# Performance work log

Hardware: AMD Instinct MI355X
Metric: run time of the kernel (lower is better)

Reference implementation:

```python
import jax, jax.numpy as jnp
import numpy as np

IN_F = 4096
OUT_F = 4096
BITS = 8
EPS = 1e-5
BATCH, SEQ = 4, 2048


def setup_inputs() -> dict:
    key = jax.random.key(0)
    k1, k2, k3 = jax.random.split(key, 3)
    bound = 1.0 / np.sqrt(IN_F)
    x = jax.random.normal(k1, (BATCH, SEQ, IN_F), dtype=jnp.float32)
    weight = jax.random.uniform(k2, (OUT_F, IN_F), dtype=jnp.float32, minval=-bound, maxval=bound)
    bias = jax.random.uniform(k3, (OUT_F,), dtype=jnp.float32, minval=-bound, maxval=bound)
    return {"x": x, "weight": weight, "bias": bias}


def _ste_round_clip(v, lo, hi):
    # round+clip with straight-through estimator
    q = jnp.clip(jnp.round(v), lo, hi)
    return v + jax.lax.stop_gradient(q - v)


def reference(x, weight, bias):
    q = jnp.float32(2 ** (BITS - 1))  # 128 for int8
    # weight ternarization: absmean scale, round to {-1,0,1}
    w_scale = jnp.maximum(jnp.mean(jnp.abs(weight)), EPS)
    w_q = _ste_round_clip(weight / w_scale, -1.0, 1.0)  # ternary [O,I]
    # activation int8 quantization: absmax scale over whole tensor (dim=None)
    gamma = jnp.maximum(jnp.max(jnp.abs(x)), EPS)
    x_q = _ste_round_clip(x * (q / gamma), -q, q - 1.0)  # int8 range values
    # integer-domain matmul then dequantize
    out = jnp.einsum('bsi,oi->bso', x_q, w_q) * (gamma * w_scale / q)
    return out + bias
```

## Files before the change

kernel.cpp:

```cpp
#include <hip/hip_runtime.h>
#include <stdint.h>

#define GLOBAL_AS __attribute__((address_space(1)))
#define LDS_AS __attribute__((address_space(3)))

typedef int v4i  __attribute__((ext_vector_type(4)));
typedef int v16i __attribute__((ext_vector_type(16)));

static constexpr int M = 8192;
static constexpr int N = 4096;
static constexpr int K = 4096;
static constexpr float F_EPS = 1e-5f;


__global__ void reduce_kernel(const float4* __restrict__ x, const float4* __restrict__ w,
                              float* __restrict__ pmax, double* __restrict__ psum) {
    const int b = blockIdx.x;
    const int t = threadIdx.x;
    if (b < 2048) {
        float m = 0.f;
        const int n4 = M * K / 4;
        int i = b * 512 + t;
        for (; i + 256 < n4; i += 2048 * 512) {
            float4 v0 = x[i];
            float4 v1 = x[i + 256];
            m = fmaxf(m, fmaxf(fmaxf(fabsf(v0.x), fabsf(v0.y)), fmaxf(fabsf(v0.z), fabsf(v0.w))));
            m = fmaxf(m, fmaxf(fmaxf(fabsf(v1.x), fabsf(v1.y)), fmaxf(fabsf(v1.z), fabsf(v1.w))));
        }
#pragma unroll
        for (int off = 32; off > 0; off >>= 1) m = fmaxf(m, __shfl_down(m, off, 64));
        __shared__ float red[4];
        if ((t & 63) == 0) red[t >> 6] = m;
        __syncthreads();
        if (t == 0) pmax[b] = fmaxf(fmaxf(red[0], red[1]), fmaxf(red[2], red[3]));
    } else {
        double s = 0.0;
        const int n4 = N * K / 4;
        int i = (b - 2048) * 512 + t;
        for (; i + 256 < n4; i += 1024 * 512) {
            float4 v0 = w[i];
            float4 v1 = w[i + 256];
            s += (double)fabsf(v0.x) + (double)fabsf(v0.y) + (double)fabsf(v0.z) + (double)fabsf(v0.w);
            s += (double)fabsf(v1.x) + (double)fabsf(v1.y) + (double)fabsf(v1.z) + (double)fabsf(v1.w);
        }
#pragma unroll
        for (int off = 32; off > 0; off >>= 1) s += __shfl_down(s, off, 64);
        __shared__ double dred[4];
        if ((t & 63) == 0) dred[t >> 6] = s;
        __syncthreads();
        if (t == 0) psum[b - 2048] = dred[0] + dred[1] + dred[2] + dred[3];
    }
}

__global__ void quant_kernel(const float4* __restrict__ x, const float4* __restrict__ w,
                             int* __restrict__ xq, int* __restrict__ wq,
                             const float* __restrict__ pmax, const double* __restrict__ psum,
                             float* __restrict__ wssc) {
    const int b = blockIdx.x;
    const int t = threadIdx.x;
    __shared__ float red[4];
    __shared__ double dred[4];
    __shared__ float sc[2];
    {
        float m = 0.f;
#pragma unroll
        for (int j = 0; j < 8; ++j) m = fmaxf(m, pmax[t + j * 256]);
        double s = psum[t] + psum[t + 256] + psum[t + 512] + psum[t + 768];
#pragma unroll
        for (int off = 32; off > 0; off >>= 1) {
            m = fmaxf(m, __shfl_down(m, off, 64));
            s += __shfl_down(s, off, 64);
        }
        if ((t & 63) == 0) { red[t >> 6] = m; dred[t >> 6] = s; }
        __syncthreads();
        if (t == 0) {
            float gamma = fmaxf(fmaxf(fmaxf(red[0], red[1]), fmaxf(red[2], red[3])), F_EPS);
            double sum = dred[0] + dred[1] + dred[2] + dred[3];
            float wscale = (float)fmax(sum * (1.0 / ((double)N * (double)K)), (double)F_EPS);
            sc[0] = 128.f / gamma;
            sc[1] = wscale;
            if (b == 0) {
                wssc[0] = 128.f / gamma;
                wssc[1] = wscale;
                wssc[2] = gamma * wscale / 128.f;
            }
        }
        __syncthreads();
    }
    const float sx = sc[0];
    const float ws = sc[1];

    if (b < 2048) {
        const int n4 = M * K / 4;
        int i = b * 512 + t;
        for (; i + 256 < n4; i += 2048 * 512) {
            float4 v0 = x[i];
            float4 v1 = x[i + 256];
            int a0 = min(127, max(-128, (int)rintf(v0.x * sx)));
            int a1 = min(127, max(-128, (int)rintf(v0.y * sx)));
            int a2 = min(127, max(-128, (int)rintf(v0.z * sx)));
            int a3 = min(127, max(-128, (int)rintf(v0.w * sx)));
            xq[i] = (a0 & 255) | ((a1 & 255) << 8) | ((a2 & 255) << 16) | (a3 << 24);
            int b0 = min(127, max(-128, (int)rintf(v1.x * sx)));
            int b1 = min(127, max(-128, (int)rintf(v1.y * sx)));
            int b2 = min(127, max(-128, (int)rintf(v1.z * sx)));
            int b3 = min(127, max(-128, (int)rintf(v1.w * sx)));
            xq[i + 256] = (b0 & 255) | ((b1 & 255) << 8) | ((b2 & 255) << 16) | (b3 << 24);
        }
    } else {
        const int n4 = N * K / 4;
        int i = (b - 2048) * 512 + t;
        for (; i + 256 < n4; i += 1024 * 512) {
            float4 v0 = w[i];
            float4 v1 = w[i + 256];
            int a0 = min(1, max(-1, (int)rintf(v0.x / ws)));
            int a1 = min(1, max(-1, (int)rintf(v0.y / ws)));
            int a2 = min(1, max(-1, (int)rintf(v0.z / ws)));
            int a3 = min(1, max(-1, (int)rintf(v0.w / ws)));
            wq[i] = (a0 & 255) | ((a1 & 255) << 8) | ((a2 & 255) << 16) | (a3 << 24);
            int b0 = min(1, max(-1, (int)rintf(v1.x / ws)));
            int b1 = min(1, max(-1, (int)rintf(v1.y / ws)));
            int b2 = min(1, max(-1, (int)rintf(v1.z / ws)));
            int b3 = min(1, max(-1, (int)rintf(v1.w / ws)));
            wq[i + 256] = (b0 & 255) | ((b1 & 255) << 8) | ((b2 & 255) << 16) | (b3 << 24);
        }
    }
}

__global__ __launch_bounds__(512, 2) void gemm_kernel(
    const int8_t* __restrict__ xq, const int8_t* __restrict__ wq,
    const float* __restrict__ bias, const float* __restrict__ wssc,
    float* __restrict__ out) {

    __shared__ __align__(16) int8_t As[4][256 * 64];
    __shared__ __align__(16) int8_t Bs[4][256 * 64];

    const int t = threadIdx.x;
    const int lane = t & 63;
    const int wv = t >> 6;
    const int half = lane >> 5;
    const int lr = lane & 31;
    const int wm0 = (wv >> 2) * 128;
    const int wn0 = (wv & 3) * 64;

    const int bid = blockIdx.x;
    const int xcd = bid & 7;
    const int cix = bid >> 3;
    const int m0 = ((xcd >> 1) * 8 + (cix >> 3)) * 256;
    const int n0 = ((xcd & 1) * 8 + (cix & 7)) * 256;

    const GLOBAL_AS int8_t* aSrc[2];
    const GLOBAL_AS int8_t* bSrc[2];
    int aLds[2], bLds[2];
#pragma unroll
    for (int j = 0; j < 2; ++j) {
        int idx = j * 512 + t;
        int c = idx >> 6;
        int s = idx & 63;
        int k = s >> 4;
        int rho = ((s & 15) - 4 * k) & 15;
        int row = c * 16 + rho;
        aSrc[j] = (const GLOBAL_AS int8_t*)(xq + (size_t)(m0 + row) * K + k * 16);
        bSrc[j] = (const GLOBAL_AS int8_t*)(wq + (size_t)(n0 + row) * K + k * 16);
        aLds[j] = idx * 16;
        bLds[j] = idx * 16;
    }

    int aOff[2][4], bOff[2][2];
#pragma unroll
    for (int ks = 0; ks < 2; ++ks) {
        int k = ks * 2 + half;
#pragma unroll
        for (int q = 0; q < 4; ++q) {
            int r = wm0 + q * 32 + lr;
            aOff[ks][q] = (r >> 4) * 1024 + k * 256 + (((r & 15) + 4 * k) & 15) * 16;
        }
#pragma unroll
        for (int q = 0; q < 2; ++q) {
            int r = wn0 + q * 32 + lr;
            bOff[ks][q] = (r >> 4) * 1024 + k * 256 + (((r & 15) + 4 * k) & 15) * 16;
        }
    }

    v16i acc[4][2];
#pragma unroll
    for (int mt = 0; mt < 4; ++mt)
#pragma unroll
        for (int nt = 0; nt < 2; ++nt)
#pragma unroll
            for (int e = 0; e < 16; ++e) acc[mt][nt][e] = 0;

    auto stage = [&](int kt, int8_t* A, int8_t* B) {
#pragma unroll
        for (int j = 0; j < 2; ++j)
            __builtin_amdgcn_global_load_lds((const GLOBAL_AS void*)(aSrc[j] + kt),
                                             (LDS_AS void*)(A + aLds[j]), 16, 0, 0);
#pragma unroll
        for (int j = 0; j < 2; ++j)
            __builtin_amdgcn_global_load_lds((const GLOBAL_AS void*)(bSrc[j] + kt),
                                             (LDS_AS void*)(B + bLds[j]), 16, 0, 0);
    };

    auto compute = [&](const int8_t* A, const int8_t* B) {
#pragma unroll
        for (int ks = 0; ks < 2; ++ks) {
            v4i a[4], b[2];
#pragma unroll
            for (int q = 0; q < 4; ++q) a[q] = *(const v4i*)(A + aOff[ks][q]);
#pragma unroll
            for (int q = 0; q < 2; ++q) b[q] = *(const v4i*)(B + bOff[ks][q]);
            __builtin_amdgcn_s_setprio(1);
#pragma unroll
            for (int mt = 0; mt < 4; ++mt)
#pragma unroll
                for (int nt = 0; nt < 2; ++nt)
                    acc[mt][nt] = __builtin_amdgcn_mfma_i32_32x32x32_i8(a[mt], b[nt], acc[mt][nt], 0, 0, 0);
            __builtin_amdgcn_s_setprio(0);
        }
    };

#define FENCE() asm volatile("" ::: "memory")
#define PIPE_STEP(NB, CB, KT)                                        \
    do {                                                             \
        stage((KT) * 64, As[NB], Bs[NB]);                            \
        asm volatile("s_waitcnt vmcnt(12)" ::: "memory");            \
        __builtin_amdgcn_s_barrier();                                \
        FENCE();                                                     \
        compute(As[CB], Bs[CB]);                                     \
        FENCE();                                                     \
        __builtin_amdgcn_s_barrier();                                \
        FENCE();                                                     \
    } while (0)

    stage(0, As[0], Bs[0]);
    stage(64, As[1], Bs[1]);
    stage(128, As[2], Bs[2]);

#pragma unroll 1
    for (int tb = 0; tb < 56; tb += 4) {
        PIPE_STEP(3, 0, tb + 3);
        PIPE_STEP(0, 1, tb + 4);
        PIPE_STEP(1, 2, tb + 5);
        PIPE_STEP(2, 3, tb + 6);
    }
    PIPE_STEP(3, 0, 59);
    PIPE_STEP(0, 1, 60);
    PIPE_STEP(1, 2, 61);
    PIPE_STEP(2, 3, 62);
    PIPE_STEP(3, 0, 63);
    asm volatile("s_waitcnt vmcnt(8)" ::: "memory");
    __builtin_amdgcn_s_barrier(); FENCE();
    compute(As[1], Bs[1]); FENCE();
    __builtin_amdgcn_s_barrier(); FENCE();
    asm volatile("s_waitcnt vmcnt(4)" ::: "memory");
    __builtin_amdgcn_s_barrier(); FENCE();
    compute(As[2], Bs[2]); FENCE();
    __builtin_amdgcn_s_barrier(); FENCE();
    asm volatile("s_waitcnt vmcnt(0)" ::: "memory");
    __builtin_amdgcn_s_barrier(); FENCE();
    compute(As[3], Bs[3]);
#undef PIPE_STEP
#undef FENCE

    const float scale = wssc[2];
#pragma unroll
    for (int nt = 0; nt < 2; ++nt) {
        int col = n0 + wn0 + nt * 32 + lr;
        float bv = bias[col];
#pragma unroll
        for (int mt = 0; mt < 4; ++mt) {
            int rb = m0 + wm0 + mt * 32 + 4 * half;
#pragma unroll
            for (int reg = 0; reg < 16; ++reg) {
                int row = rb + (reg & 3) + 8 * (reg >> 2);
                out[(size_t)row * N + col] = (float)acc[mt][nt][reg] * scale + bv;
            }
        }
    }
}

extern "C" void kernel_launch(void* const* d_in, const int* in_sizes, int n_in,
                              void* d_out, int out_size, void* d_ws, size_t ws_size,
                              hipStream_t stream) {
    const float* x = (const float*)d_in[0];
    const float* w = (const float*)d_in[1];
    const float* bias = (const float*)d_in[2];
    float* out = (float*)d_out;

    float* wssc = (float*)d_ws;
    float* pmax = (float*)((char*)d_ws + 256);
    double* psum = (double*)((char*)d_ws + 8448);
    int8_t* xq = (int8_t*)d_ws + 16640;
    int8_t* wq = xq + (size_t)M * K;

    hipLaunchKernelGGL(reduce_kernel, dim3(3072), dim3(256), 0, stream,
                       (const float4*)x, (const float4*)w, pmax, psum);
    hipLaunchKernelGGL(quant_kernel, dim3(3072), dim3(256), 0, stream,
                       (const float4*)x, (const float4*)w, (int*)xq, (int*)wq,
                       pmax, psum, wssc);
    hipLaunchKernelGGL(gemm_kernel, dim3(512), dim3(512), 0, stream,
                       xq, wq, bias, wssc, out);
}
```

Baseline: 460.2 us.

## Restructure int8 GEMM main loop into fine-grained interleaved phases with ping-pong buffers

Replaces the 4-stage per-tile pipeline (stage, wait, compute 16 MFMAs, barrier) with a finer 8-phase schedule per pair of K-tiles. Each phase loads 4 LDS fragments, issues one global_load_lds, barriers, then runs 4 MFMAs. Buffers are used as two ping-pong pairs. The aim is to spread global loads evenly among MFMA groups and interleave LDS reads with compute, hiding latency better. The cost is many more barriers per K-tile, and the prefetch distance changes from three tiles to roughly two.

```diff
diff --git a/kernel.cpp b/kernel.cpp
--- a/kernel.cpp
+++ b/kernel.cpp
@@ -190,77 +190,85 @@
 #pragma unroll
             for (int e = 0; e < 16; ++e) acc[mt][nt][e] = 0;
 
-    auto stage = [&](int kt, int8_t* A, int8_t* B) {
-#pragma unroll
-        for (int j = 0; j < 2; ++j)
-            __builtin_amdgcn_global_load_lds((const GLOBAL_AS void*)(aSrc[j] + kt),
-                                             (LDS_AS void*)(A + aLds[j]), 16, 0, 0);
-#pragma unroll
-        for (int j = 0; j < 2; ++j)
-            __builtin_amdgcn_global_load_lds((const GLOBAL_AS void*)(bSrc[j] + kt),
-                                             (LDS_AS void*)(B + bLds[j]), 16, 0, 0);
-    };
-
-    auto compute = [&](const int8_t* A, const int8_t* B) {
-#pragma unroll
-        for (int ks = 0; ks < 2; ++ks) {
-            v4i a[4], b[2];
-#pragma unroll
-            for (int q = 0; q < 4; ++q) a[q] = *(const v4i*)(A + aOff[ks][q]);
-#pragma unroll
-            for (int q = 0; q < 2; ++q) b[q] = *(const v4i*)(B + bOff[ks][q]);
-            __builtin_amdgcn_s_setprio(1);
-#pragma unroll
-            for (int mt = 0; mt < 4; ++mt)
-#pragma unroll
-                for (int nt = 0; nt < 2; ++nt)
-                    acc[mt][nt] = __builtin_amdgcn_mfma_i32_32x32x32_i8(a[mt], b[nt], acc[mt][nt], 0, 0, 0);
-            __builtin_amdgcn_s_setprio(0);
-        }
-    };
-
-#define FENCE() asm volatile("" ::: "memory")
-#define PIPE_STEP(NB, CB, KT)                                        \
-    do {                                                             \
-        stage((KT) * 64, As[NB], Bs[NB]);                            \
-        asm volatile("s_waitcnt vmcnt(12)" ::: "memory");            \
-        __builtin_amdgcn_s_barrier();                                \
-        FENCE();                                                     \
-        compute(As[CB], Bs[CB]);                                     \
-        FENCE();                                                     \
-        __builtin_amdgcn_s_barrier();                                \
-        FENCE();                                                     \
+#define GL(SRC, DST) __builtin_amdgcn_global_load_lds((const GLOBAL_AS void*)(SRC), \
+                                                      (LDS_AS void*)(DST), 16, 0, 0)
+#define MFMA_I8(A_, B_, C_) __builtin_amdgcn_mfma_i32_32x32x32_i8(A_, B_, C_, 0, 0, 0)
+
+#define PHASE(Ab, Bb, KS, MH, STAGE_STMT, WAIT_STMT)                        \
+    do {                                                                    \
+        const v4i a0_ = *(const v4i*)((Ab) + aOff[KS][2 * (MH)]);           \
+        const v4i a1_ = *(const v4i*)((Ab) + aOff[KS][2 * (MH) + 1]);       \
+        const v4i b0_ = *(const v4i*)((Bb) + bOff[KS][0]);                  \
+        const v4i b1_ = *(const v4i*)((Bb) + bOff[KS][1]);                  \
+        STAGE_STMT;                                                         \
+        asm volatile("" ::: "memory");                                      \
+        __builtin_amdgcn_s_barrier();                                       \
+        asm volatile("s_waitcnt lgkmcnt(0)" ::: "memory");                  \
+        __builtin_amdgcn_sched_barrier(0);                                  \
+        __builtin_amdgcn_s_setprio(1);                                      \
+        acc[2 * (MH)][0] = MFMA_I8(a0_, b0_, acc[2 * (MH)][0]);             \
+        acc[2 * (MH)][1] = MFMA_I8(a0_, b1_, acc[2 * (MH)][1]);             \
+        acc[2 * (MH) + 1][0] = MFMA_I8(a1_, b0_, acc[2 * (MH) + 1][0]);     \
+        acc[2 * (MH) + 1][1] = MFMA_I8(a1_, b1_, acc[2 * (MH) + 1][1]);     \
+        __builtin_amdgcn_s_setprio(0);                                      \
+        WAIT_STMT;                                                          \
+        asm volatile("" ::: "memory");                                      \
+        __builtin_amdgcn_s_barrier();                                       \
     } while (0)
 
-    stage(0, As[0], Bs[0]);
-    stage(64, As[1], Bs[1]);
-    stage(128, As[2], Bs[2]);
+#define VM4  asm volatile("s_waitcnt vmcnt(4)" ::: "memory")
+#define VM0  asm volatile("s_waitcnt vmcnt(0)" ::: "memory")
+#define NOP  ((void)0)
+
+    GL(aSrc[0] + 0,  As[0] + aLds[0]);
+    GL(aSrc[1] + 0,  As[0] + aLds[1]);
+    GL(bSrc[0] + 0,  Bs[0] + bLds[0]);
+    GL(bSrc[1] + 0,  Bs[0] + bLds[1]);
+    GL(aSrc[0] + 64, As[1] + aLds[0]);
+    GL(aSrc[1] + 64, As[1] + aLds[1]);
+    GL(bSrc[0] + 64, Bs[1] + bLds[0]);
+    GL(bSrc[1] + 64, Bs[1] + bLds[1]);
+    VM4;
+    asm volatile("" ::: "memory");
+    __builtin_amdgcn_s_barrier();
 
 #pragma unroll 1
-    for (int tb = 0; tb < 56; tb += 4) {
-        PIPE_STEP(3, 0, tb + 3);
-        PIPE_STEP(0, 1, tb + 4);
-        PIPE_STEP(1, 2, tb + 5);
-        PIPE_STEP(2, 3, tb + 6);
-    }
-    PIPE_STEP(3, 0, 59);
-    PIPE_STEP(0, 1, 60);
-    PIPE_STEP(1, 2, 61);
-    PIPE_STEP(2, 3, 62);
-    PIPE_STEP(3, 0, 63);
-    asm volatile("s_waitcnt vmcnt(8)" ::: "memory");
-    __builtin_amdgcn_s_barrier(); FENCE();
-    compute(As[1], Bs[1]); FENCE();
-    __builtin_amdgcn_s_barrier(); FENCE();
-    asm volatile("s_waitcnt vmcnt(4)" ::: "memory");
-    __builtin_amdgcn_s_barrier(); FENCE();
-    compute(As[2], Bs[2]); FENCE();
-    __builtin_amdgcn_s_barrier(); FENCE();
-    asm volatile("s_waitcnt vmcnt(0)" ::: "memory");
-    __builtin_amdgcn_s_barrier(); FENCE();
-    compute(As[3], Bs[3]);
-#undef PIPE_STEP
-#undef FENCE
+    for (int it = 0; it < 31; ++it) {
+        const int pc = it & 1;
+        const int pn = pc ^ 1;
+        const int8_t* A0 = As[pc * 2 + 0];
+        const int8_t* B0 = Bs[pc * 2 + 0];
+        const int8_t* A1 = As[pc * 2 + 1];
+        const int8_t* B1 = Bs[pc * 2 + 1];
+        int8_t* dA0 = As[pn * 2 + 0];
+        int8_t* dB0 = Bs[pn * 2 + 0];
+        int8_t* dA1 = As[pn * 2 + 1];
+        int8_t* dB1 = Bs[pn * 2 + 1];
+        const int kt2 = (2 * it + 2) * 64;
+        const int kt3 = kt2 + 64;
+        PHASE(A0, B0, 0, 0, GL(aSrc[0] + kt2, dA0 + aLds[0]), NOP);
+        PHASE(A0, B0, 0, 1, GL(aSrc[1] + kt2, dA0 + aLds[1]), NOP);
+        PHASE(A0, B0, 1, 0, GL(bSrc[0] + kt2, dB0 + bLds[0]), NOP);
+        PHASE(A0, B0, 1, 1, GL(bSrc[1] + kt2, dB0 + bLds[1]), VM4);
+        PHASE(A1, B1, 0, 0, GL(aSrc[0] + kt3, dA1 + aLds[0]), NOP);
+        PHASE(A1, B1, 0, 1, GL(aSrc[1] + kt3, dA1 + aLds[1]), NOP);
+        PHASE(A1, B1, 1, 0, GL(bSrc[0] + kt3, dB1 + bLds[0]), NOP);
+        PHASE(A1, B1, 1, 1, GL(bSrc[1] + kt3, dB1 + bLds[1]), VM4);
+    }
+    PHASE(As[2], Bs[2], 0, 0, NOP, NOP);
+    PHASE(As[2], Bs[2], 0, 1, NOP, NOP);
+    PHASE(As[2], Bs[2], 1, 0, NOP, NOP);
+    PHASE(As[2], Bs[2], 1, 1, NOP, VM0);
+    PHASE(As[3], Bs[3], 0, 0, NOP, NOP);
+    PHASE(As[3], Bs[3], 0, 1, NOP, NOP);
+    PHASE(As[3], Bs[3], 1, 0, NOP, NOP);
+    PHASE(As[3], Bs[3], 1, 1, NOP, NOP);
+#undef PHASE
+#undef VM4
+#undef VM0
+#undef NOP
+#undef GL
+#undef MFMA_I8
 
     const float scale = wssc[2];
 #pragma unroll
```

Measured after the change: 483.5 us. +5.1%, slower.
